# Performance work log

Measured on AMD Instinct MI355X. Metric: run time of the kernel, lower is better.

Reference implementation:

```python
import jax, jax.numpy as jnp
import numpy as np

N_NODES = 50000
N_EDGES = 1600000
D_EDGE = 64
D_VERT = 64
D_IN = D_EDGE + 2 * D_VERT  # 192
D_HID = 128
D_OUT = 64


def setup_inputs() -> dict:
    key = jax.random.key(0)
    ks = jax.random.split(key, 8)
    edata = jax.random.normal(ks[0], (N_EDGES, D_EDGE), dtype=jnp.float32)
    vfeat = jax.random.normal(ks[1], (N_NODES, D_VERT), dtype=jnp.float32)
    W1 = jax.random.normal(ks[2], (D_IN, D_HID), dtype=jnp.float32) * (1.0 / np.sqrt(D_IN))
    b1 = jnp.zeros((D_HID,), dtype=jnp.float32)
    W2 = jax.random.normal(ks[3], (D_HID, D_OUT), dtype=jnp.float32) * (1.0 / np.sqrt(D_HID))
    b2 = jnp.zeros((D_OUT,), dtype=jnp.float32)
    senders = jax.random.randint(ks[4], (N_EDGES,), 0, N_NODES, dtype=jnp.int64)
    receivers = jax.random.randint(ks[5], (N_EDGES,), 0, N_NODES, dtype=jnp.int64)
    return {"edata": edata, "vfeat": vfeat, "W1": W1, "b1": b1,
            "W2": W2, "b2": b2, "senders": senders, "receivers": receivers}


def reference(edata, vfeat, W1, b1, W2, b2, senders, receivers):
    # Per-edge gather of receiver/sender vertex features, concat with edge
    # features (matches torch.cat([edata[e], v[recv], v[send]]) per edge,
    # vectorized), then updater MLP: Linear -> ReLU -> Linear.
    x = jnp.concatenate([edata, vfeat[receivers], vfeat[senders]], axis=-1)  # [E, 192]
    h = jax.nn.relu(x @ W1 + b1)  # [E, 128]
    return h @ W2 + b2            # [E, 64]
```

## Files before the change

kernel.cpp:

```cpp
#include <hip/hip_runtime.h>
#include <hip/hip_bf16.h>

#define E_TOTAL   1600000
#define NV        50000
#define DE        64
#define DV        64
#define DIN       192
#define DHID      128
#define DOUT      64
#define TILE_M    64
#define XS        200
#define HS        136
#define NTILES    (E_TOTAL / TILE_M)

typedef __bf16 bf16x8 __attribute__((ext_vector_type(8)));
typedef float  floatx4 __attribute__((ext_vector_type(4)));
typedef float  fx4     __attribute__((ext_vector_type(4)));

static __device__ __forceinline__ unsigned short f2bf(float f) {
    unsigned int u = __float_as_uint(f);
    u += 0x7fffu + ((u >> 16) & 1u);
    return (unsigned short)(u >> 16);
}

__global__ void prep_kernel(const float* __restrict__ W1, const float* __restrict__ W2,
                            const float* __restrict__ vfeat,
                            unsigned short* __restrict__ w1t,
                            unsigned short* __restrict__ w2t,
                            unsigned short* __restrict__ vfb, int do_vfb) {
    int tid = blockIdx.x * blockDim.x + threadIdx.x;
    int stride = gridDim.x * blockDim.x;
    for (int i = tid; i < DIN * DHID; i += stride) {
        int n = i / DIN, k = i % DIN;
        w1t[i] = f2bf(W1[k * DHID + n]);
    }
    for (int i = tid; i < DHID * DOUT; i += stride) {
        int n = i / DHID, k = i % DHID;
        w2t[i] = f2bf(W2[k * DOUT + n]);
    }
    if (do_vfb) {
        const fx4* src = (const fx4*)vfeat;
        ushort4* dst = (ushort4*)vfb;
        int n4 = NV * DV / 4;
        for (int i = tid; i < n4; i += stride) {
            fx4 v = src[i];
            ushort4 o;
            o.x = f2bf(v[0]); o.y = f2bf(v[1]); o.z = f2bf(v[2]); o.w = f2bf(v[3]);
            dst[i] = o;
        }
    }
}

template <bool USE_VFB>
__global__ __launch_bounds__(256, 2) void edge_mlp(
    const float* __restrict__ edata,
    const float* __restrict__ vfeat,
    const float* __restrict__ b1,
    const float* __restrict__ b2,
    const int* __restrict__ senders,
    const int* __restrict__ receivers,
    const unsigned short* __restrict__ w1t,
    const unsigned short* __restrict__ w2t,
    const unsigned short* __restrict__ vfb,
    float* __restrict__ out) {
    __shared__ unsigned short xb[TILE_M * XS];
    __shared__ unsigned short hb[TILE_M * HS];

    const int tid  = threadIdx.x;
    const int lane = tid & 63;
    const int wave = tid >> 6;
    const int l15  = lane & 15;
    const int quad = lane >> 4;

    bf16x8 w1f[6][2];
    bf16x8 w2f[4];
    {
        for (int nb = 0; nb < 2; ++nb) {
            int n = wave * 32 + nb * 16 + l15;
            const unsigned short* p = w1t + n * DIN + quad * 8;
            for (int ks = 0; ks < 6; ++ks)
                w1f[ks][nb] = *(const bf16x8*)(p + ks * 32);
        }
        int n2 = wave * 16 + l15;
        const unsigned short* p2 = w2t + n2 * DHID + quad * 8;
        for (int ks = 0; ks < 4; ++ks)
            w2f[ks] = *(const bf16x8*)(p2 + ks * 32);
    }
    const float bias1a = b1[wave * 32 + l15];
    const float bias1b = b1[wave * 32 + 16 + l15];
    const float bias2  = b2[wave * 16 + l15];

    for (int t = blockIdx.x; t < NTILES; t += gridDim.x) {
        const int e0 = t * TILE_M;

        {
#pragma unroll
            for (int it = 0; it < 4; ++it) {
                int idx = it * 256 + tid;
                int e = idx >> 4;
                int c = idx & 15;
                fx4 v = __builtin_nontemporal_load((const fx4*)(edata + (e0 + e) * DE + c * 4));
                ushort4 o;
                o.x = f2bf(v[0]); o.y = f2bf(v[1]); o.z = f2bf(v[2]); o.w = f2bf(v[3]);
                *(ushort4*)(xb + e * XS + c * 4) = o;
            }
            if constexpr (USE_VFB) {
#pragma unroll
                for (int it = 0; it < 4; ++it) {
                    int idx = it * 256 + tid;
                    int e = idx >> 4;
                    int g = (idx >> 3) & 1;
                    int c = idx & 7;
                    int row = g ? senders[e0 + e] : receivers[e0 + e];
                    uint4 v = *(const uint4*)(vfb + row * DV + c * 8);
                    *(uint4*)(xb + e * XS + DE + g * DV + c * 8) = v;
                }
            } else {
#pragma unroll
                for (int it = 0; it < 8; ++it) {
                    int idx = it * 256 + tid;
                    int e = idx >> 5;
                    int g = (idx >> 4) & 1;
                    int c = idx & 15;
                    int row = g ? senders[e0 + e] : receivers[e0 + e];
                    fx4 v = *(const fx4*)(vfeat + row * DV + c * 4);
                    ushort4 o;
                    o.x = f2bf(v[0]); o.y = f2bf(v[1]); o.z = f2bf(v[2]); o.w = f2bf(v[3]);
                    *(ushort4*)(xb + e * XS + DE + g * DV + c * 4) = o;
                }
            }
        }
        __syncthreads();

        floatx4 acc[4][2];
#pragma unroll
        for (int mb = 0; mb < 4; ++mb) {
            acc[mb][0] = (floatx4){bias1a, bias1a, bias1a, bias1a};
            acc[mb][1] = (floatx4){bias1b, bias1b, bias1b, bias1b};
        }
#pragma unroll
        for (int ks = 0; ks < 6; ++ks) {
            bf16x8 a[4];
#pragma unroll
            for (int mb = 0; mb < 4; ++mb)
                a[mb] = *(const bf16x8*)(xb + (mb * 16 + l15) * XS + ks * 32 + quad * 8);
#pragma unroll
            for (int mb = 0; mb < 4; ++mb)
#pragma unroll
                for (int nb = 0; nb < 2; ++nb)
                    acc[mb][nb] = __builtin_amdgcn_mfma_f32_16x16x32_bf16(
                        a[mb], w1f[ks][nb], acc[mb][nb], 0, 0, 0);
        }
#pragma unroll
        for (int mb = 0; mb < 4; ++mb) {
            int rowm = mb * 16 + quad * 4;
#pragma unroll
            for (int nb = 0; nb < 2; ++nb) {
                int col = wave * 32 + nb * 16 + l15;
#pragma unroll
                for (int r = 0; r < 4; ++r) {
                    float v = acc[mb][nb][r];
                    v = v > 0.f ? v : 0.f;
                    hb[(rowm + r) * HS + col] = f2bf(v);
                }
            }
        }
        __syncthreads();

        floatx4 acc2[4];
#pragma unroll
        for (int mb = 0; mb < 4; ++mb)
            acc2[mb] = (floatx4){bias2, bias2, bias2, bias2};
#pragma unroll
        for (int ks = 0; ks < 4; ++ks)
#pragma unroll
            for (int mb = 0; mb < 4; ++mb) {
                bf16x8 a2 = *(const bf16x8*)(hb + (mb * 16 + l15) * HS + ks * 32 + quad * 8);
                acc2[mb] = __builtin_amdgcn_mfma_f32_16x16x32_bf16(a2, w2f[ks], acc2[mb], 0, 0, 0);
            }
#pragma unroll
        for (int mb = 0; mb < 4; ++mb) {
            int rowm = mb * 16 + quad * 4;
            int col = wave * 16 + l15;
#pragma unroll
            for (int r = 0; r < 4; ++r)
                __builtin_nontemporal_store(acc2[mb][r], out + (e0 + rowm + r) * DOUT + col);
        }
        __syncthreads();
    }
}

extern "C" void kernel_launch(void* const* d_in, const int* in_sizes, int n_in,
                              void* d_out, int out_size, void* d_ws, size_t ws_size,
                              hipStream_t stream) {
    const float* edata     = (const float*)d_in[0];
    const float* vfeat     = (const float*)d_in[1];
    const float* W1        = (const float*)d_in[2];
    const float* b1        = (const float*)d_in[3];
    const float* W2        = (const float*)d_in[4];
    const float* b2        = (const float*)d_in[5];
    const int*   senders   = (const int*)d_in[6];
    const int*   receivers = (const int*)d_in[7];
    float* out = (float*)d_out;

    unsigned short* w1t = (unsigned short*)d_ws;
    unsigned short* w2t = w1t + DIN * DHID;
    unsigned short* vfb = w2t + DHID * DOUT;
    const size_t need_vfb = (size_t)(DIN * DHID + DHID * DOUT + NV * DV) * sizeof(unsigned short);
    const bool use_vfb = ws_size >= need_vfb;

    prep_kernel<<<512, 256, 0, stream>>>(W1, W2, vfeat, w1t, w2t, vfb, use_vfb ? 1 : 0);
    if (use_vfb)
        edge_mlp<true><<<1536, 256, 0, stream>>>(edata, vfeat, b1, b2, senders, receivers,
                                                 w1t, w2t, vfb, out);
    else
        edge_mlp<false><<<1536, 256, 0, stream>>>(edata, vfeat, b1, b2, senders, receivers,
                                                  w1t, w2t, vfb, out);
}
```

Baseline: 717.2 us.

## Software-pipeline next tile's loads and swap MFMA operands for vectorized stores

Restructures the persistent tile loop so the next tile's index and edge-feature loads are issued before the current tile's first GEMM, and the vertex gather is issued before the second GEMM. The staged registers are written to LDS only after the current tile finishes, which hides global-memory latency behind MFMA work. MFMA A/B operands are swapped so the accumulator layout is transposed. That lets the hidden-activation and output writes use 4-wide vector stores instead of scalar ones, and bias is loaded per-row accordingly. It also adds s_setprio around the MFMA loops and hardware bf16 conversions. The cost is higher register pressure under launch_bounds(256,2), which risks spills or lower occupancy.

After: 767.6 us. 1.07x slower.

```diff
diff --git a/kernel.cpp b/kernel.cpp
--- a/kernel.cpp
+++ b/kernel.cpp
@@ -13,7 +13,8 @@
 #define HS        136
 #define NTILES    (E_TOTAL / TILE_M)
 
-typedef __bf16 bf16x8 __attribute__((ext_vector_type(8)));
+typedef __bf16 bf16x8  __attribute__((ext_vector_type(8)));
+typedef __bf16 bf16x4  __attribute__((ext_vector_type(4)));
 typedef float  floatx4 __attribute__((ext_vector_type(4)));
 typedef float  fx4     __attribute__((ext_vector_type(4)));
 
@@ -86,58 +87,122 @@
         for (int ks = 0; ks < 4; ++ks)
             w2f[ks] = *(const bf16x8*)(p2 + ks * 32);
     }
-    const float bias1a = b1[wave * 32 + l15];
-    const float bias1b = b1[wave * 32 + 16 + l15];
-    const float bias2  = b2[wave * 16 + l15];
-
-    for (int t = blockIdx.x; t < NTILES; t += gridDim.x) {
-        const int e0 = t * TILE_M;
-
-        {
+    float b1v[2][4], b2v[4];
+#pragma unroll
+    for (int nb = 0; nb < 2; ++nb)
+#pragma unroll
+        for (int r = 0; r < 4; ++r)
+            b1v[nb][r] = b1[wave * 32 + nb * 16 + quad * 4 + r];
+#pragma unroll
+    for (int r = 0; r < 4; ++r)
+        b2v[r] = b2[wave * 16 + quad * 4 + r];
+
+    int   rix[4];
+    fx4   ed[4];
+    uint4 gv[4];
+    int   rix8[8];
+    fx4   gf[8];
+
+    auto issue_idx = [&](long eb) {
+        if constexpr (USE_VFB) {
 #pragma unroll
             for (int it = 0; it < 4; ++it) {
                 int idx = it * 256 + tid;
-                int e = idx >> 4;
+                int e = idx >> 4, g = (idx >> 3) & 1;
+                rix[it] = (g ? senders : receivers)[eb + e];
+            }
+        } else {
+#pragma unroll
+            for (int it = 0; it < 8; ++it) {
+                int idx = it * 256 + tid;
+                int e = idx >> 5, g = (idx >> 4) & 1;
+                rix8[it] = (g ? senders : receivers)[eb + e];
+            }
+        }
+    };
+    auto issue_edata = [&](long eb) {
+#pragma unroll
+        for (int it = 0; it < 4; ++it) {
+            int idx = it * 256 + tid;
+            int e = idx >> 4, c = idx & 15;
+            ed[it] = __builtin_nontemporal_load((const fx4*)(edata + (eb + e) * DE + c * 4));
+        }
+    };
+    auto issue_gather = [&]() {
+        if constexpr (USE_VFB) {
+#pragma unroll
+            for (int it = 0; it < 4; ++it) {
+                int idx = it * 256 + tid;
+                int c = idx & 7;
+                gv[it] = *(const uint4*)(vfb + rix[it] * DV + c * 8);
+            }
+        } else {
+#pragma unroll
+            for (int it = 0; it < 8; ++it) {
+                int idx = it * 256 + tid;
                 int c = idx & 15;
-                fx4 v = __builtin_nontemporal_load((const fx4*)(edata + (e0 + e) * DE + c * 4));
-                ushort4 o;
-                o.x = f2bf(v[0]); o.y = f2bf(v[1]); o.z = f2bf(v[2]); o.w = f2bf(v[3]);
-                *(ushort4*)(xb + e * XS + c * 4) = o;
-            }
-            if constexpr (USE_VFB) {
-#pragma unroll
-                for (int it = 0; it < 4; ++it) {
-                    int idx = it * 256 + tid;
-                    int e = idx >> 4;
-                    int g = (idx >> 3) & 1;
-                    int c = idx & 7;
-                    int row = g ? senders[e0 + e] : receivers[e0 + e];
-                    uint4 v = *(const uint4*)(vfb + row * DV + c * 8);
-                    *(uint4*)(xb + e * XS + DE + g * DV + c * 8) = v;
-                }
-            } else {
-#pragma unroll
-                for (int it = 0; it < 8; ++it) {
-                    int idx = it * 256 + tid;
-                    int e = idx >> 5;
-                    int g = (idx >> 4) & 1;
-                    int c = idx & 15;
-                    int row = g ? senders[e0 + e] : receivers[e0 + e];
-                    fx4 v = *(const fx4*)(vfeat + row * DV + c * 4);
-                    ushort4 o;
-                    o.x = f2bf(v[0]); o.y = f2bf(v[1]); o.z = f2bf(v[2]); o.w = f2bf(v[3]);
-                    *(ushort4*)(xb + e * XS + DE + g * DV + c * 4) = o;
-                }
-            }
-        }
-        __syncthreads();
+                gf[it] = *(const fx4*)(vfeat + (long)rix8[it] * DV + c * 4);
+            }
+        }
+    };
+    auto write_xb = [&]() {
+#pragma unroll
+        for (int it = 0; it < 4; ++it) {
+            int idx = it * 256 + tid;
+            int e = idx >> 4, c = idx & 15;
+            fx4 v = ed[it];
+            bf16x4 o;
+            o[0] = (__bf16)v[0]; o[1] = (__bf16)v[1];
+            o[2] = (__bf16)v[2]; o[3] = (__bf16)v[3];
+            *(bf16x4*)(xb + e * XS + c * 4) = o;
+        }
+        if constexpr (USE_VFB) {
+#pragma unroll
+            for (int it = 0; it < 4; ++it) {
+                int idx = it * 256 + tid;
+                int e = idx >> 4, g = (idx >> 3) & 1, c = idx & 7;
+                *(uint4*)(xb + e * XS + DE + g * DV + c * 8) = gv[it];
+            }
+        } else {
+#pragma unroll
+            for (int it = 0; it < 8; ++it) {
+                int idx = it * 256 + tid;
+                int e = idx >> 5, g = (idx >> 4) & 1, c = idx & 15;
+                fx4 v = gf[it];
+                bf16x4 o;
+                o[0] = (__bf16)v[0]; o[1] = (__bf16)v[1];
+                o[2] = (__bf16)v[2]; o[3] = (__bf16)v[3];
+                *(bf16x4*)(xb + e * XS + DE + g * DV + c * 4) = o;
+            }
+        }
+    };
+
+    int t = blockIdx.x;
+
+    issue_idx((long)t * TILE_M);
+    issue_edata((long)t * TILE_M);
+    issue_gather();
+    write_xb();
+    __syncthreads();
+
+    while (true) {
+        const long eb0 = (long)t * TILE_M;
+        const int tn = t + (int)gridDim.x;
+        const bool has_next = tn < NTILES;
+
+        if (has_next) {
+            issue_idx((long)tn * TILE_M);
+            issue_edata((long)tn * TILE_M);
+            __builtin_amdgcn_sched_barrier(0);
+        }
 
         floatx4 acc[4][2];
 #pragma unroll
-        for (int mb = 0; mb < 4; ++mb) {
-            acc[mb][0] = (floatx4){bias1a, bias1a, bias1a, bias1a};
-            acc[mb][1] = (floatx4){bias1b, bias1b, bias1b, bias1b};
-        }
+        for (int mb = 0; mb < 4; ++mb)
+#pragma unroll
+            for (int nb = 0; nb < 2; ++nb)
+                acc[mb][nb] = (floatx4){b1v[nb][0], b1v[nb][1], b1v[nb][2], b1v[nb][3]};
+        __builtin_amdgcn_s_setprio(1);
 #pragma unroll
         for (int ks = 0; ks < 6; ++ks) {
             bf16x8 a[4];
@@ -149,44 +214,54 @@
 #pragma unroll
                 for (int nb = 0; nb < 2; ++nb)
                     acc[mb][nb] = __builtin_amdgcn_mfma_f32_16x16x32_bf16(
-                        a[mb], w1f[ks][nb], acc[mb][nb], 0, 0, 0);
-        }
-#pragma unroll
-        for (int mb = 0; mb < 4; ++mb) {
-            int rowm = mb * 16 + quad * 4;
+                        w1f[ks][nb], a[mb], acc[mb][nb], 0, 0, 0);
+        }
+        __builtin_amdgcn_s_setprio(0);
+
+#pragma unroll
+        for (int mb = 0; mb < 4; ++mb)
 #pragma unroll
             for (int nb = 0; nb < 2; ++nb) {
-                int col = wave * 32 + nb * 16 + l15;
+                bf16x4 o;
 #pragma unroll
                 for (int r = 0; r < 4; ++r) {
                     float v = acc[mb][nb][r];
-                    v = v > 0.f ? v : 0.f;
-                    hb[(rowm + r) * HS + col] = f2bf(v);
+                    o[r] = (__bf16)(v > 0.f ? v : 0.f);
                 }
-            }
-        }
+                *(bf16x4*)(hb + (mb * 16 + l15) * HS + wave * 32 + nb * 16 + quad * 4) = o;
+            }
+
+        if (has_next) {
+            issue_gather();
+            __builtin_amdgcn_sched_barrier(0);
+        }
+
         __syncthreads();
 
         floatx4 acc2[4];
 #pragma unroll
         for (int mb = 0; mb < 4; ++mb)
-            acc2[mb] = (floatx4){bias2, bias2, bias2, bias2};
+            acc2[mb] = (floatx4){b2v[0], b2v[1], b2v[2], b2v[3]};
+        __builtin_amdgcn_s_setprio(1);
 #pragma unroll
         for (int ks = 0; ks < 4; ++ks)
 #pragma unroll
             for (int mb = 0; mb < 4; ++mb) {
                 bf16x8 a2 = *(const bf16x8*)(hb + (mb * 16 + l15) * HS + ks * 32 + quad * 8);
-                acc2[mb] = __builtin_amdgcn_mfma_f32_16x16x32_bf16(a2, w2f[ks], acc2[mb], 0, 0, 0);
-            }
-#pragma unroll
-        for (int mb = 0; mb < 4; ++mb) {
-            int rowm = mb * 16 + quad * 4;
-            int col = wave * 16 + l15;
-#pragma unroll
-            for (int r = 0; r < 4; ++r)
-                __builtin_nontemporal_store(acc2[mb][r], out + (e0 + rowm + r) * DOUT + col);
-        }
+                acc2[mb] = __builtin_amdgcn_mfma_f32_16x16x32_bf16(w2f[ks], a2, acc2[mb], 0, 0, 0);
+            }
+        __builtin_amdgcn_s_setprio(0);
+
+#pragma unroll
+        for (int mb = 0; mb < 4; ++mb)
+            __builtin_nontemporal_store(acc2[mb],
+                (fx4*)(out + (eb0 + mb * 16 + l15) * DOUT + wave * 16 + quad * 4));
+
+        if (!has_next) break;
+
+        write_xb();
         __syncthreads();
+        t = tn;
     }
 }
 
```

## Transpose MFMA operands so accumulators hold row-contiguous outputs and vectorize stores

Applied to the files above, without the earlier changes.

Swaps the A/B operands of both MFMAs so each lane's accumulator holds 4 consecutive output columns of one row instead of 4 rows of one column. Hidden activations can then be written to LDS as 8-byte bf16x4 stores, and outputs go to global memory as 16-byte vector stores instead of scalar nontemporal stores. It also uses native bf16 conversion instead of manual rounding, drops the trailing barrier, and widens the edge offset to 64-bit. Removing the end-of-tile barrier relies on the next iteration's first barrier to keep the hb reads and writes ordered.

New measurement: 821.1 us. +14.5%, slower.

```diff
diff --git a/kernel.cpp b/kernel.cpp
--- a/kernel.cpp
+++ b/kernel.cpp
@@ -13,7 +13,8 @@
 #define HS        136
 #define NTILES    (E_TOTAL / TILE_M)
 
-typedef __bf16 bf16x8 __attribute__((ext_vector_type(8)));
+typedef __bf16 bf16x8  __attribute__((ext_vector_type(8)));
+typedef __bf16 bf16x4  __attribute__((ext_vector_type(4)));
 typedef float  floatx4 __attribute__((ext_vector_type(4)));
 typedef float  fx4     __attribute__((ext_vector_type(4)));
 
@@ -86,12 +87,18 @@
         for (int ks = 0; ks < 4; ++ks)
             w2f[ks] = *(const bf16x8*)(p2 + ks * 32);
     }
-    const float bias1a = b1[wave * 32 + l15];
-    const float bias1b = b1[wave * 32 + 16 + l15];
-    const float bias2  = b2[wave * 16 + l15];
+    float b1v[2][4], b2v[4];
+#pragma unroll
+    for (int nb = 0; nb < 2; ++nb)
+#pragma unroll
+        for (int r = 0; r < 4; ++r)
+            b1v[nb][r] = b1[wave * 32 + nb * 16 + quad * 4 + r];
+#pragma unroll
+    for (int r = 0; r < 4; ++r)
+        b2v[r] = b2[wave * 16 + quad * 4 + r];
 
     for (int t = blockIdx.x; t < NTILES; t += gridDim.x) {
-        const int e0 = t * TILE_M;
+        const long e0 = (long)t * TILE_M;
 
         {
 #pragma unroll
@@ -100,9 +107,10 @@
                 int e = idx >> 4;
                 int c = idx & 15;
                 fx4 v = __builtin_nontemporal_load((const fx4*)(edata + (e0 + e) * DE + c * 4));
-                ushort4 o;
-                o.x = f2bf(v[0]); o.y = f2bf(v[1]); o.z = f2bf(v[2]); o.w = f2bf(v[3]);
-                *(ushort4*)(xb + e * XS + c * 4) = o;
+                bf16x4 o;
+                o[0] = (__bf16)v[0]; o[1] = (__bf16)v[1];
+                o[2] = (__bf16)v[2]; o[3] = (__bf16)v[3];
+                *(bf16x4*)(xb + e * XS + c * 4) = o;
             }
             if constexpr (USE_VFB) {
 #pragma unroll
@@ -123,10 +131,11 @@
                     int g = (idx >> 4) & 1;
                     int c = idx & 15;
                     int row = g ? senders[e0 + e] : receivers[e0 + e];
-                    fx4 v = *(const fx4*)(vfeat + row * DV + c * 4);
-                    ushort4 o;
-                    o.x = f2bf(v[0]); o.y = f2bf(v[1]); o.z = f2bf(v[2]); o.w = f2bf(v[3]);
-                    *(ushort4*)(xb + e * XS + DE + g * DV + c * 4) = o;
+                    fx4 v = *(const fx4*)(vfeat + (long)row * DV + c * 4);
+                    bf16x4 o;
+                    o[0] = (__bf16)v[0]; o[1] = (__bf16)v[1];
+                    o[2] = (__bf16)v[2]; o[3] = (__bf16)v[3];
+                    *(bf16x4*)(xb + e * XS + DE + g * DV + c * 4) = o;
                 }
             }
         }
@@ -134,10 +143,10 @@
 
         floatx4 acc[4][2];
 #pragma unroll
-        for (int mb = 0; mb < 4; ++mb) {
-            acc[mb][0] = (floatx4){bias1a, bias1a, bias1a, bias1a};
-            acc[mb][1] = (floatx4){bias1b, bias1b, bias1b, bias1b};
-        }
+        for (int mb = 0; mb < 4; ++mb)
+#pragma unroll
+            for (int nb = 0; nb < 2; ++nb)
+                acc[mb][nb] = (floatx4){b1v[nb][0], b1v[nb][1], b1v[nb][2], b1v[nb][3]};
 #pragma unroll
         for (int ks = 0; ks < 6; ++ks) {
             bf16x8 a[4];
@@ -149,44 +158,38 @@
 #pragma unroll
                 for (int nb = 0; nb < 2; ++nb)
                     acc[mb][nb] = __builtin_amdgcn_mfma_f32_16x16x32_bf16(
-                        a[mb], w1f[ks][nb], acc[mb][nb], 0, 0, 0);
-        }
-#pragma unroll
-        for (int mb = 0; mb < 4; ++mb) {
-            int rowm = mb * 16 + quad * 4;
+                        w1f[ks][nb], a[mb], acc[mb][nb], 0, 0, 0);
+        }
+
+#pragma unroll
+        for (int mb = 0; mb < 4; ++mb)
 #pragma unroll
             for (int nb = 0; nb < 2; ++nb) {
-                int col = wave * 32 + nb * 16 + l15;
+                bf16x4 o;
 #pragma unroll
                 for (int r = 0; r < 4; ++r) {
                     float v = acc[mb][nb][r];
-                    v = v > 0.f ? v : 0.f;
-                    hb[(rowm + r) * HS + col] = f2bf(v);
+                    o[r] = (__bf16)(v > 0.f ? v : 0.f);
                 }
-            }
-        }
+                *(bf16x4*)(hb + (mb * 16 + l15) * HS + wave * 32 + nb * 16 + quad * 4) = o;
+            }
         __syncthreads();
 
         floatx4 acc2[4];
 #pragma unroll
         for (int mb = 0; mb < 4; ++mb)
-            acc2[mb] = (floatx4){bias2, bias2, bias2, bias2};
+            acc2[mb] = (floatx4){b2v[0], b2v[1], b2v[2], b2v[3]};
 #pragma unroll
         for (int ks = 0; ks < 4; ++ks)
 #pragma unroll
             for (int mb = 0; mb < 4; ++mb) {
                 bf16x8 a2 = *(const bf16x8*)(hb + (mb * 16 + l15) * HS + ks * 32 + quad * 8);
-                acc2[mb] = __builtin_amdgcn_mfma_f32_16x16x32_bf16(a2, w2f[ks], acc2[mb], 0, 0, 0);
-            }
-#pragma unroll
-        for (int mb = 0; mb < 4; ++mb) {
-            int rowm = mb * 16 + quad * 4;
-            int col = wave * 16 + l15;
-#pragma unroll
-            for (int r = 0; r < 4; ++r)
-                __builtin_nontemporal_store(acc2[mb][r], out + (e0 + rowm + r) * DOUT + col);
-        }
-        __syncthreads();
+                acc2[mb] = __builtin_amdgcn_mfma_f32_16x16x32_bf16(w2f[ks], a2, acc2[mb], 0, 0, 0);
+            }
+
+#pragma unroll
+        for (int mb = 0; mb < 4; ++mb)
+            *(fx4*)(out + (e0 + mb * 16 + l15) * DOUT + wave * 16 + quad * 4) = acc2[mb];
     }
 }
 
```
